# Optimization experiments

Hardware: AMD Instinct MI355X
Metric: run time of the kernel (lower is better)

Reference implementation:

```python
import jax, jax.numpy as jnp
import numpy as np


def setup_inputs() -> dict:
    key0 = jax.random.key(0)
    k1, k2, k3, k4 = jax.random.split(key0, 4)
    B, T, S, QK, V = 4, 4096, 4096, 1, 512
    query = jax.random.normal(k1, (B, T, QK), dtype=jnp.float32)
    key = jax.random.normal(k2, (B, S, QK), dtype=jnp.float32)
    value = jax.random.normal(k3, (B, V, S), dtype=jnp.float32)
    log_scale = jnp.asarray(0.0, dtype=jnp.float32)  # nn.Parameter(init_log_scale=0.0)
    return {"query": query, "key": key, "value": value, "log_scale": log_scale}


def _distance(a, b):
    # a: [B,N,X], b: [B,M,X] -> [B,N,M]
    if a.shape[-1] == 1 and b.shape[-1] == 1:
        return (a - jnp.swapaxes(b, 1, 2)) ** 2
    a_norm = jnp.sum(a ** 2, axis=-1)[..., :, None]
    b_norm = jnp.sum(b ** 2, axis=-1)[..., None, :]
    return a_norm + b_norm - 2.0 * jnp.einsum('bnx,bmx->bnm', a, b)


def reference(query, key, value, log_scale):
    # weight = exp(-0.5 * dist(key, query) / exp(2*log_scale))  : [B,S,T]
    dist = _distance(key, query)
    weight = jnp.exp(-0.5 * dist / jnp.exp(2.0 * log_scale))
    # value [B,V,S] @ weight [B,S,T] -> [B,V,T]
    out = jnp.einsum('bvs,bst->bvt', value, weight)
    # dim_last=True -> transpose(-2,-1): [B,T,V]
    return jnp.swapaxes(out, -2, -1)
```

## Files before the change

### kernel.cpp

```cpp
#include <hip/hip_runtime.h>

typedef unsigned short u16;
typedef __attribute__((ext_vector_type(8))) short short8;
typedef __attribute__((ext_vector_type(4))) float f32x4;

#define X0    (-6.0f)
#define GH    (12.0f / 256.0f)
#define LOG2E 1.44269504089f

__device__ __forceinline__ unsigned int cvtpk(float lo, float hi) {
    unsigned int r;
    asm("v_cvt_pk_bf16_f32 %0, %1, %2" : "=v"(r) : "v"(lo), "v"(hi));
    return r;
}
__device__ __forceinline__ uint4 cvt8u(float4 lo, float4 hi) {
    return make_uint4(cvtpk(lo.x, lo.y), cvtpk(lo.z, lo.w),
                      cvtpk(hi.x, hi.y), cvtpk(hi.z, hi.w));
}
__device__ __forceinline__ u16 f2bf(float x) {
    return (u16)(cvtpk(x, x) & 0xffffu);
}
__device__ __forceinline__ float bf2f_lo(unsigned int u) {
    union { unsigned int x; float f; } v; v.x = u << 16; return v.f;
}
__device__ __forceinline__ float bf2f_hi(unsigned int u) {
    union { unsigned int x; float f; } v; v.x = u & 0xffff0000u; return v.f;
}
__device__ __forceinline__ void glds16(const float* g, const float* l) {
    __builtin_amdgcn_global_load_lds(
        (const __attribute__((address_space(1))) void*)g,
        (__attribute__((address_space(3))) void*)l, 16, 0, 0);
}

__global__ __launch_bounds__(256) void hpart_kernel(
    const float* __restrict__ key, const float* __restrict__ value,
    u16* __restrict__ Hpart)
{
    __shared__ float Vt[16 * 1024];
    __shared__ float tl[512];

    const int tid   = threadIdx.x;
    const int v0    = blockIdx.x << 5;
    const int b     = blockIdx.y;
    const int ks    = blockIdx.z;
    const int kbase = ks << 9;
    const int lane  = tid & 63;
    const int wave  = tid >> 6;
    const int wj    = wave << 6;
    const int m15   = lane & 15;
    const int kq    = lane >> 4;

    #pragma unroll
    for (int r = 0; r < 2; ++r) {
        int s = tid + (r << 8);
        float k = key[b * 4096 + kbase + s];
        float u = (k - X0) * (256.0f / 12.0f);
        int j = (int)floorf(u);
        j = j < 0 ? 0 : (j > 254 ? 254 : j);
        float f = u - (float)j;
        f = f < 0.0f ? 0.0f : (f > 1.0f ? 1.0f : f);
        tl[s] = (float)j + f;
    }

    const int srow = tid >> 3;
    const int scs  = (tid & 7) ^ (srow & 7);
    const float* gsrc = value + (size_t)(b * 512 + v0 + srow) * 4096 + kbase
                              + (scs << 2);
    const float* ldst = Vt + (srow << 5) + ((tid & 7) << 2);
    #pragma unroll
    for (int kk = 0; kk < 16; ++kk)
        glds16(gsrc + (kk << 5), ldst + (kk << 10));

    f32x4 acc[2][4];
    #pragma unroll
    for (int i = 0; i < 2; ++i)
        #pragma unroll
        for (int j = 0; j < 4; ++j)
            acc[i][j] = (f32x4){0.f, 0.f, 0.f, 0.f};

    __syncthreads();

    for (int kk = 0; kk < 16; ++kk) {
        const float* Vk = Vt + (kk << 10);

        union U { short8 s; uint4 u; } af[2];
        #pragma unroll
        for (int mi = 0; mi < 2; ++mi) {
            int m  = mi * 16 + m15;
            int c0 = ((2 * kq)     ^ (m & 7)) << 2;
            int c1 = ((2 * kq + 1) ^ (m & 7)) << 2;
            float4 lo = *(const float4*)(Vk + (m << 5) + c0);
            float4 hi = *(const float4*)(Vk + (m << 5) + c1);
            af[mi].u = cvt8u(lo, hi);
        }

        float ts[8];
        #pragma unroll
        for (int i = 0; i < 8; ++i)
            ts[i] = tl[(kk << 5) + (kq << 3) + i];

        #pragma unroll
        for (int ni = 0; ni < 4; ++ni) {
            const float J = (float)(wj + ni * 16 + m15);
            float w[8];
            #pragma unroll
            for (int i = 0; i < 8; ++i) {
                float d = 1.0f - fabsf(J - ts[i]);
                w[i] = d > 0.0f ? d : 0.0f;
            }
            union U bf;
            bf.u = cvt8u(make_float4(w[0], w[1], w[2], w[3]),
                         make_float4(w[4], w[5], w[6], w[7]));
            #pragma unroll
            for (int mi = 0; mi < 2; ++mi)
                acc[mi][ni] = __builtin_amdgcn_mfma_f32_16x16x32_bf16(
                    af[mi].s, bf.s, acc[mi][ni], 0, 0, 0);
        }
    }

    #pragma unroll
    for (int mi = 0; mi < 2; ++mi)
        #pragma unroll
        for (int ni = 0; ni < 4; ++ni) {
            #pragma unroll
            for (int r = 0; r < 4; ++r) {
                int v = v0 + mi * 16 + (kq << 2) + r;
                Hpart[((size_t)(b * 8 + ks) * 512 + v) * 256
                      + wj + ni * 16 + m15] = f2bf(acc[mi][ni][r]);
            }
        }
}

__global__ __launch_bounds__(256) void hred_kernel(
    const u16* __restrict__ Hpart, u16* __restrict__ Hbf)
{
    const int gid  = blockIdx.x * 256 + threadIdx.x;
    const int b    = gid >> 14;
    const size_t off8 = (size_t)(gid & 16383) * 8;
    float s[8];
    #pragma unroll
    for (int i = 0; i < 8; ++i) s[i] = 0.f;
    #pragma unroll
    for (int ks = 0; ks < 8; ++ks) {
        const u16* p = Hpart + (size_t)(b * 8 + ks) * 131072 + off8;
        uint4 a = *(const uint4*)p;
        s[0] += bf2f_lo(a.x); s[1] += bf2f_hi(a.x);
        s[2] += bf2f_lo(a.y); s[3] += bf2f_hi(a.y);
        s[4] += bf2f_lo(a.z); s[5] += bf2f_hi(a.z);
        s[6] += bf2f_lo(a.w); s[7] += bf2f_hi(a.w);
    }
    *(uint4*)(Hbf + (size_t)b * 131072 + off8) =
        cvt8u(make_float4(s[0], s[1], s[2], s[3]),
              make_float4(s[4], s[5], s[6], s[7]));
}

__global__ __launch_bounds__(256) void gemm_kernel(
    const float* __restrict__ query, const float* __restrict__ log_scale,
    const u16* __restrict__ Hbf, float* __restrict__ out)
{
    extern __shared__ u16 Hl[];

    const int tid  = threadIdx.x;
    const int v0   = blockIdx.x << 7;
    const int t0   = blockIdx.y << 7;
    const int b    = blockIdx.z;
    const int lane = tid & 63;
    const int wave = tid >> 6;
    const int wv   = (wave & 1) << 6;
    const int wt   = (wave >> 1) << 6;
    const int m15  = lane & 15;
    const int kq   = lane >> 4;

    const float c2   = -0.5f * LOG2E * exp2f(-2.0f * LOG2E * log_scale[0]);
    const float rho  = exp2f(2.0f * c2 * GH * GH);
    const float c2h2 = c2 * GH * GH;
    const float A    = 2.0f * c2 * GH;

    float q[4];
    for (int ni = 0; ni < 4; ++ni)
        q[ni] = query[b * 4096 + t0 + wt + ni * 16 + m15];

    {
        const int row = tid >> 1, half = tid & 1;
        const u16* src = Hbf + (size_t)(b * 512 + v0 + row) * 256 + half * 128;
        u16* dst = Hl + row * 264 + half * 128;
        #pragma unroll
        for (int i = 0; i < 16; ++i)
            *(uint4*)(dst + i * 8) = *(const uint4*)(src + i * 8);
    }
    __syncthreads();

    f32x4 acc[4][4];
    for (int i = 0; i < 4; ++i)
        for (int j = 0; j < 4; ++j)
            acc[i][j] = (f32x4){0.f, 0.f, 0.f, 0.f};

    for (int ks = 0; ks < 8; ++ks) {
        const int k0 = ks << 5;
        short8 af[4];
        for (int i = 0; i < 4; ++i)
            af[i] = *(const short8*)(Hl + (wv + i * 16 + m15) * 264 + k0 + kq * 8);

        const float xb = X0 + GH * (float)(k0 + kq * 8);

        short8 bfr[4];
        #pragma unroll
        for (int ni = 0; ni < 4; ++ni) {
            float d0 = q[ni] - xb;
            float e  = exp2f(c2 * d0 * d0);
            float r  = exp2f(c2h2 - A * d0);
            float w[8];
            #pragma unroll
            for (int j = 0; j < 8; ++j) {
                w[j] = e;
                e *= r;
                r *= rho;
            }
            union U { short8 s; uint4 u; } v;
            v.u = cvt8u(make_float4(w[0], w[1], w[2], w[3]),
                        make_float4(w[4], w[5], w[6], w[7]));
            bfr[ni] = v.s;
        }
        for (int mi = 0; mi < 4; ++mi)
            for (int ni = 0; ni < 4; ++ni)
                acc[mi][ni] = __builtin_amdgcn_mfma_f32_16x16x32_bf16(
                    af[mi], bfr[ni], acc[mi][ni], 0, 0, 0);
    }

    for (int mi = 0; mi < 4; ++mi)
        for (int ni = 0; ni < 4; ++ni) {
            int t = t0 + wt + ni * 16 + m15;
            float* o = out + (size_t)(b * 4096 + t) * 512
                           + v0 + wv + mi * 16 + (kq << 2);
            *(f32x4*)o = acc[mi][ni];
        }
}

extern "C" void kernel_launch(void* const* d_in, const int* in_sizes, int n_in,
                              void* d_out, int out_size, void* d_ws, size_t ws_size,
                              hipStream_t stream)
{
    const float* query = (const float*)d_in[0];
    const float* key   = (const float*)d_in[1];
    const float* value = (const float*)d_in[2];
    const float* lsc   = (const float*)d_in[3];
    float* out = (float*)d_out;

    u16* Hpart = (u16*)d_ws;
    u16* Hbf   = (u16*)((char*)d_ws + (size_t)8 * 1024 * 1024);

    hpart_kernel<<<dim3(16, 4, 8), 256, 0, stream>>>(key, value, Hpart);
    hred_kernel<<<256, 256, 0, stream>>>(Hpart, Hbf);
    gemm_kernel<<<dim3(4, 32, 4), 256, 128 * 264 * 2, stream>>>(query, lsc, Hbf, out);
}
```

Baseline: 118.6 us.

## Scatter sparse hat-weight B tiles into LDS and pre-convert values to bf16

The hpart kernel no longer evaluates the dense triangular hat weight for every (grid node, key) pair. Each key lane now scatters its two nonzero bf16 weights into a per-wave zeroed LDS tile, the MFMA B fragments are read from that tile, and the entries are cleared again afterwards. The value tile is loaded into registers, converted to bf16 once and stored to LDS with an XOR swizzle, which replaces the async global-to-LDS fp32 copy and the per-iteration conversion. In exchange the code adds LDS scatter stores, extra LDS traffic and register pressure, and depends on wave-level ordering between the scatter, the fragment reads and the clears without a barrier.

```diff
diff --git a/kernel.cpp b/kernel.cpp
--- a/kernel.cpp
+++ b/kernel.cpp
@@ -26,18 +26,14 @@
 __device__ __forceinline__ float bf2f_hi(unsigned int u) {
     union { unsigned int x; float f; } v; v.x = u & 0xffff0000u; return v.f;
 }
-__device__ __forceinline__ void glds16(const float* g, const float* l) {
-    __builtin_amdgcn_global_load_lds(
-        (const __attribute__((address_space(1))) void*)g,
-        (__attribute__((address_space(3))) void*)l, 16, 0, 0);
-}
 
 __global__ __launch_bounds__(256) void hpart_kernel(
     const float* __restrict__ key, const float* __restrict__ value,
     u16* __restrict__ Hpart)
 {
-    __shared__ float Vt[16 * 1024];
-    __shared__ float tl[512];
+    __shared__ u16    Vt[16 * 1024];
+    __shared__ float2 jf[512];
+    __shared__ u16    bt[4][64 * 32];
 
     const int tid   = threadIdx.x;
     const int v0    = blockIdx.x << 5;
@@ -59,17 +55,35 @@
         j = j < 0 ? 0 : (j > 254 ? 254 : j);
         float f = u - (float)j;
         f = f < 0.0f ? 0.0f : (f > 1.0f ? 1.0f : f);
-        tl[s] = (float)j + f;
-    }
-
-    const int srow = tid >> 3;
-    const int scs  = (tid & 7) ^ (srow & 7);
-    const float* gsrc = value + (size_t)(b * 512 + v0 + srow) * 4096 + kbase
-                              + (scs << 2);
-    const float* ldst = Vt + (srow << 5) + ((tid & 7) << 2);
-    #pragma unroll
-    for (int kk = 0; kk < 16; ++kk)
-        glds16(gsrc + (kk << 5), ldst + (kk << 10));
+        jf[s] = make_float2((float)j, f);
+    }
+
+    {
+        const int row = tid >> 3, g = tid & 7;
+        const float* gv = value + (size_t)(b * 512 + v0 + row) * 4096 + kbase
+                                + (g << 2);
+        float4 ld[16];
+        #pragma unroll
+        for (int kk = 0; kk < 16; ++kk)
+            ld[kk] = *(const float4*)(gv + (kk << 5));
+        const int ch = ((g >> 1) ^ ((row >> 1) & 3));
+        u16* dst0 = Vt + (row << 5) + (ch << 3) + ((g & 1) << 2);
+        #pragma unroll
+        for (int kk = 0; kk < 16; ++kk) {
+            uint2 w;
+            w.x = cvtpk(ld[kk].x, ld[kk].y);
+            w.y = cvtpk(ld[kk].z, ld[kk].w);
+            *(uint2*)(dst0 + (kk << 10)) = w;
+        }
+    }
+
+    u16* myb = bt[wave];
+    {
+        uint4 z = make_uint4(0u, 0u, 0u, 0u);
+        #pragma unroll
+        for (int zz = 0; zz < 4; ++zz)
+            *(uint4*)(myb + (lane << 5) + (zz << 3)) = z;
+    }
 
     f32x4 acc[2][4];
     #pragma unroll
@@ -80,41 +94,44 @@
 
     __syncthreads();
 
+    const bool wr = (lane < 32);
+
     for (int kk = 0; kk < 16; ++kk) {
-        const float* Vk = Vt + (kk << 10);
-
-        union U { short8 s; uint4 u; } af[2];
+        short8 af[2];
         #pragma unroll
         for (int mi = 0; mi < 2; ++mi) {
-            int m  = mi * 16 + m15;
-            int c0 = ((2 * kq)     ^ (m & 7)) << 2;
-            int c1 = ((2 * kq + 1) ^ (m & 7)) << 2;
-            float4 lo = *(const float4*)(Vk + (m << 5) + c0);
-            float4 hi = *(const float4*)(Vk + (m << 5) + c1);
-            af[mi].u = cvt8u(lo, hi);
-        }
-
-        float ts[8];
-        #pragma unroll
-        for (int i = 0; i < 8; ++i)
-            ts[i] = tl[(kk << 5) + (kq << 3) + i];
-
-        #pragma unroll
-        for (int ni = 0; ni < 4; ++ni) {
-            const float J = (float)(wj + ni * 16 + m15);
-            float w[8];
-            #pragma unroll
-            for (int i = 0; i < 8; ++i) {
-                float d = 1.0f - fabsf(J - ts[i]);
-                w[i] = d > 0.0f ? d : 0.0f;
-            }
-            union U bf;
-            bf.u = cvt8u(make_float4(w[0], w[1], w[2], w[3]),
-                         make_float4(w[4], w[5], w[6], w[7]));
+            int m = mi * 16 + m15;
+            af[mi] = *(const short8*)(Vt + (kk << 10) + (m << 5)
+                                      + ((kq ^ ((m >> 1) & 3)) << 3));
+        }
+
+        int r0 = -1, r1 = -1; int a0, a1; unsigned pkw = 0;
+        if (wr) {
+            float2 p = jf[(kk << 5) + lane];
+            int j   = (int)p.x;
+            float f = p.y;
+            pkw = cvtpk(1.0f - f, f);
+            r0 = j - wj; r1 = r0 + 1;
+            a0 = (r0 << 5) + (((lane >> 3) ^ ((r0 >> 1) & 3)) << 3) + (lane & 7);
+            a1 = (r1 << 5) + (((lane >> 3) ^ ((r1 >> 1) & 3)) << 3) + (lane & 7);
+            if (r0 >= 0 && r0 < 64) myb[a0] = (u16)(pkw & 0xffffu);
+            if (r1 >= 0 && r1 < 64) myb[a1] = (u16)(pkw >> 16);
+        }
+
+        #pragma unroll
+        for (int ni = 0; ni < 4; ++ni) {
+            int Jr = ni * 16 + m15;
+            short8 bf = *(const short8*)(myb + (Jr << 5)
+                                         + ((kq ^ ((Jr >> 1) & 3)) << 3));
             #pragma unroll
             for (int mi = 0; mi < 2; ++mi)
                 acc[mi][ni] = __builtin_amdgcn_mfma_f32_16x16x32_bf16(
-                    af[mi].s, bf.s, acc[mi][ni], 0, 0, 0);
+                    af[mi], bf, acc[mi][ni], 0, 0, 0);
+        }
+
+        if (wr) {
+            if (r0 >= 0 && r0 < 64) myb[a0] = 0;
+            if (r1 >= 0 && r1 < 64) myb[a1] = 0;
         }
     }
 
```

Measured after the change: 109.2 us. 7.9% less time.
